# Optimization experiments

Measured on AMD Instinct MI355X. Metric: run time of the kernel, lower is better.

The kernel has to match this reference:

```python
import jax, jax.numpy as jnp
import numpy as np

# Residue-type multiplicative bonuses from _add_chemical_property_bonuses
# dict: {1:1.3, 3:1.2, 6:1.2, 8:1.4, 11:1.3, 13:1.5, 17:1.6, 18:1.4, 19:1.1,
#        0:1.05, 2:1.1, 5:1.1, 15:1.05, 16:1.05}, default 1.0
_BOND_TABLE = np.full(20, 1.0, dtype=np.float32)
for k, v in {1: 1.3, 3: 1.2, 6: 1.2, 8: 1.4, 11: 1.3, 13: 1.5, 17: 1.6,
             18: 1.4, 19: 1.1, 0: 1.05, 2: 1.1, 5: 1.1, 15: 1.05, 16: 1.05}.items():
    _BOND_TABLE[k] = v

DIRECT_R = 3.5    # direct contact radius (A)
EXT_R = 8.0       # extended interaction radius (A)
NEIGH_R2 = 25.0   # surface-accessibility neighbor radius squared (5 A)^2


def setup_inputs() -> dict:
    key = jax.random.key(0)
    k1, k2, k3, k4 = jax.random.split(key, 4)
    N, M, F = 16384, 64, 16
    pos = jax.random.uniform(k1, (N, 3), dtype=jnp.float32) * 40.0          # protein box
    ligand_pos = jax.random.uniform(k2, (M, 3), dtype=jnp.float32) * 10.0 + 15.0  # centered ligand
    x = jax.random.normal(k3, (N, F), dtype=jnp.float32)
    res = jax.random.randint(k4, (N,), 0, 20)
    x = x.at[:, 1].set(res.astype(jnp.float32))  # column 1 = residue type code
    return {"pos": pos, "ligand_pos": ligand_pos, "x": x, "max_atoms": 512}


def reference(pos, ligand_pos, x, max_atoms):
    # --- min distance of each pocket atom to any ligand atom: [N]
    d2l_sq = jnp.sum((pos[:, None, :] - ligand_pos[None, :, :]) ** 2, axis=-1)  # [N, M]
    min_d = jnp.sqrt(jnp.maximum(jnp.min(d2l_sq, axis=1), 1e-12))               # [N]

    direct = min_d <= DIRECT_R
    extended = (min_d > DIRECT_R) & (min_d <= EXT_R)
    far = min_d > EXT_R

    # --- surface accessibility among far atoms only (as in torch: pos[far_mask])
    # Compare squared distances (equivalent to d<5 & d>0, avoids sqrt on the NxN block).
    sq = jnp.sum((pos[:, None, :] - pos[None, :, :]) ** 2, axis=-1)  # [N, N]
    neigh = (sq < NEIGH_R2) & (sq > 0.0) & far[None, :]              # neighbors within far subset
    counts = jnp.where(far, jnp.sum(neigh, axis=1).astype(pos.dtype), 0.0)
    max_n = jnp.max(counts)
    max_n = jnp.where(max_n > 0, max_n, 1.0)
    surface = 1.0 - counts / (max_n + 1e-6)

    # --- tiered scores
    scores = jnp.where(
        direct, 10.0,
        jnp.where(extended, 5.0 * (EXT_R - min_d) / EXT_R, surface))

    # --- chemical property bonuses (vectorized lookup-table gather)
    res_type = jnp.clip(x[:, 1].astype(jnp.int32), 0, 19)
    scores = scores * jnp.asarray(_BOND_TABLE)[res_type]

    top_scores, indices = jax.lax.top_k(scores, max_atoms)
    return scores, top_scores, indices
```

## Files before the change

### kernel.cpp

```cpp
#include <hip/hip_runtime.h>
#include <stdint.h>

#define TILE 256
#define NCELLS 512
#define NHIST 2048
#define GQ 16

__device__ __constant__ float BOND[20] = {
    1.05f, 1.30f, 1.10f, 1.20f, 1.00f, 1.10f, 1.20f, 1.00f, 1.40f, 1.00f,
    1.00f, 1.30f, 1.00f, 1.50f, 1.00f, 1.05f, 1.05f, 1.60f, 1.40f, 1.10f};

__device__ __forceinline__ int clamp8(int v) { return v < 0 ? 0 : (v > 7 ? 7 : v); }

__global__ void k_init(int* __restrict__ cellCount, int* __restrict__ hist,
                       int* __restrict__ scalars) {
  int t = blockIdx.x * blockDim.x + threadIdx.x;
  int stride = blockDim.x * gridDim.x;
  for (int b = t; b < NCELLS; b += stride) cellCount[b] = 0;
  for (int b = t; b < NHIST; b += stride) hist[b] = 0;
  if (t < 4) scalars[t] = 0;
}

__global__ void k_classify(const float* __restrict__ pos, const float* __restrict__ lig,
                           float* __restrict__ minD, int* __restrict__ cellCount,
                           int N, int M) {
#pragma clang fp contract(off)
  __shared__ float sl[768];
  int t = threadIdx.x;
  for (int idx = t; idx < 3 * M; idx += blockDim.x) sl[idx] = lig[idx];
  __syncthreads();
  int i = blockIdx.x * blockDim.x + t;
  if (i >= N) return;
  float px = pos[3 * i], py = pos[3 * i + 1], pz = pos[3 * i + 2];
  float m = 3.4e38f;
  for (int j = 0; j < M; ++j) {
    float dx = px - sl[3 * j];
    float dy = py - sl[3 * j + 1];
    float dz = pz - sl[3 * j + 2];
    float d2 = dx * dx + dy * dy + dz * dz;
    m = fminf(m, d2);
  }
  float md = sqrtf(fmaxf(m, 1e-12f));
  minD[i] = md;
  if (md > 8.0f) {
    int cx = clamp8((int)(px * 0.2f));
    int cy = clamp8((int)(py * 0.2f));
    int cz = clamp8((int)(pz * 0.2f));
    atomicAdd(&cellCount[(cz * 8 + cy) * 8 + cx], 1);
  }
}

__global__ void k_scan(const int* __restrict__ cellCount, int* __restrict__ cellStart,
                       int* __restrict__ cellCursor) {
  __shared__ int s[256];
  int t = threadIdx.x;
  int c0 = cellCount[2 * t], c1 = cellCount[2 * t + 1];
  int p = c0 + c1;
  s[t] = p;
  __syncthreads();
  for (int off = 1; off < 256; off <<= 1) {
    int v = (t >= off) ? s[t - off] : 0;
    __syncthreads();
    s[t] += v;
    __syncthreads();
  }
  int excl = s[t] - p;
  cellStart[2 * t] = excl;          cellCursor[2 * t] = excl;
  cellStart[2 * t + 1] = excl + c0; cellCursor[2 * t + 1] = excl + c0;
  if (t == 255) cellStart[NCELLS] = s[255];
}

__global__ void k_scatter(const float* __restrict__ pos, const float* __restrict__ minD,
                          int* __restrict__ cellCursor, float4* __restrict__ sortedPos,
                          int N) {
  int i = blockIdx.x * blockDim.x + threadIdx.x;
  if (i >= N) return;
  if (!(minD[i] > 8.0f)) return;
  float px = pos[3 * i], py = pos[3 * i + 1], pz = pos[3 * i + 2];
  int cx = clamp8((int)(px * 0.2f));
  int cy = clamp8((int)(py * 0.2f));
  int cz = clamp8((int)(pz * 0.2f));
  int slot = atomicAdd(&cellCursor[(cz * 8 + cy) * 8 + cx], 1);
  sortedPos[slot] = make_float4(px, py, pz, __int_as_float(i));
}

__global__ void k_query(const float4* __restrict__ sortedPos,
                        const int* __restrict__ cellStart, int* __restrict__ counts,
                        int* __restrict__ scalars, int N) {
#pragma clang fp contract(off)
  int g = blockIdx.x * blockDim.x + threadIdx.x;
  int q = g / GQ;
  int lane = g & (GQ - 1);
  int F = cellStart[NCELLS];
  int cnt = 0;
  int idx = -1;
  if (q < F) {
    float4 qp = sortedPos[q];
    idx = __float_as_int(qp.w);
    int cx = clamp8((int)(qp.x * 0.2f));
    int cy = clamp8((int)(qp.y * 0.2f));
    int cz = clamp8((int)(qp.z * 0.2f));
    int x0 = cx > 0 ? cx - 1 : 0;
    int x1 = cx < 7 ? cx + 1 : 7;
    int zlo = cz > 0 ? cz - 1 : 0, zhi = cz < 7 ? cz + 1 : 7;
    int ylo = cy > 0 ? cy - 1 : 0, yhi = cy < 7 ? cy + 1 : 7;
    for (int z = zlo; z <= zhi; ++z) {
      for (int y = ylo; y <= yhi; ++y) {
        int rb = (z * 8 + y) * 8;
        int k0 = cellStart[rb + x0];
        int k1 = cellStart[rb + x1 + 1];
        for (int k = k0 + lane; k < k1; k += GQ) {
          float4 p = sortedPos[k];
          float dx = qp.x - p.x;
          float dy = qp.y - p.y;
          float dz = qp.z - p.z;
          float d2 = dx * dx + dy * dy + dz * dz;
          cnt += (d2 < 25.0f && d2 > 0.0f) ? 1 : 0;
        }
      }
    }
  }
  cnt += __shfl_xor(cnt, 1, 64);
  cnt += __shfl_xor(cnt, 2, 64);
  cnt += __shfl_xor(cnt, 4, 64);
  cnt += __shfl_xor(cnt, 8, 64);
  if (lane == 0 && q < F) counts[idx] = cnt;
  int m = cnt;
  m = max(m, __shfl_xor(m, 16, 64));
  m = max(m, __shfl_xor(m, 32, 64));
  if ((threadIdx.x & 63) == 0 && m > 0) atomicMax(&scalars[0], m);
}

__global__ void k_score(const float* __restrict__ minD, const int* __restrict__ counts,
                        const int* __restrict__ scalars, const float* __restrict__ x,
                        float* __restrict__ out_scores, uint64_t* __restrict__ keys,
                        int* __restrict__ hist, int N, int F) {
#pragma clang fp contract(off)
  __shared__ int lh[NHIST];
  for (int b = threadIdx.x; b < NHIST; b += blockDim.x) lh[b] = 0;
  __syncthreads();
  int i = blockIdx.x * blockDim.x + threadIdx.x;
  if (i < N) {
    float md = minD[i];
    float mn = (float)scalars[0];
    if (!(mn > 0.0f)) mn = 1.0f;
    float score;
    if (md <= 3.5f) {
      score = 10.0f;
    } else if (md <= 8.0f) {
      score = 5.0f * (8.0f - md) / 8.0f;
    } else {
      float cf = (float)counts[i];
      score = 1.0f - cf / (mn + 1e-6f);
    }
    int rt = (int)x[(size_t)i * F + 1];
    rt = rt < 0 ? 0 : (rt > 19 ? 19 : rt);
    score = score * BOND[rt];
    out_scores[i] = score;
    uint32_t fb = __float_as_uint(score);
    keys[i] = ((uint64_t)fb << 32) | (uint64_t)(0x7FFFFFFFu - (uint32_t)i);
    atomicAdd(&lh[fb >> 20], 1);
  }
  __syncthreads();
  for (int b = threadIdx.x; b < NHIST; b += blockDim.x) {
    int v = lh[b];
    if (v) atomicAdd(&hist[b], v);
  }
}

__global__ void k_sel(const int* __restrict__ hist, int* __restrict__ scalars, int K) {
  __shared__ int s[256];
  int t = threadIdx.x;
  int base = t * 8;
  int local = 0;
  for (int b = 0; b < 8; ++b) local += hist[base + b];
  s[t] = local;
  __syncthreads();
  for (int off = 1; off < 256; off <<= 1) {
    int v = (t + off < 256) ? s[t + off] : 0;
    __syncthreads();
    s[t] += v;
    __syncthreads();
  }
  int cumNext = (t < 255) ? s[t + 1] : 0;
  if (s[t] >= K && cumNext < K) {
    int running = cumNext;
    int B = base;
    for (int b = base + 7; b >= base; --b) {
      running += hist[b];
      if (running >= K) { B = b; break; }
    }
    scalars[2] = B;
  }
}

__global__ void k_compact(const uint64_t* __restrict__ keys, int* __restrict__ scalars,
                          uint64_t* __restrict__ cand, int N) {
  int i = blockIdx.x * blockDim.x + threadIdx.x;
  if (i >= N) return;
  uint64_t k = keys[i];
  if ((int)(k >> 52) >= scalars[2]) {
    int p = atomicAdd(&scalars[1], 1);
    cand[p] = k;
  }
}

__global__ void k_rank_emit(const uint64_t* __restrict__ cand,
                            const int* __restrict__ scalars,
                            float* __restrict__ out_top, float* __restrict__ out_idx,
                            int K) {
  int C = scalars[1];
  if (blockIdx.x * blockDim.x >= C) return;
  __shared__ uint64_t sk[TILE];
  int t = threadIdx.x;
  int g = blockIdx.x * blockDim.x + t;
  uint64_t ki = (g < C) ? cand[g] : ~0ull;
  int r = 0;
  int nt = (C + TILE - 1) / TILE;
  for (int tb = 0; tb < nt; ++tb) {
    __syncthreads();
    int j = tb * TILE + t;
    sk[t] = (j < C) ? cand[j] : 0ull;
    __syncthreads();
#pragma unroll 16
    for (int jj = 0; jj < TILE; ++jj) r += (sk[jj] > ki) ? 1 : 0;
  }
  if (g < C && r < K) {
    out_top[r] = __uint_as_float((uint32_t)(ki >> 32));
    out_idx[r] = (float)(0x7FFFFFFFu - (uint32_t)ki);
  }
}

extern "C" void kernel_launch(void* const* d_in, const int* in_sizes, int n_in,
                              void* d_out, int out_size, void* d_ws, size_t ws_size,
                              hipStream_t stream) {
  const float* pos = (const float*)d_in[0];
  const float* lig = (const float*)d_in[1];
  const float* x   = (const float*)d_in[2];
  int N = in_sizes[0] / 3;
  int M = in_sizes[1] / 3;
  int F = in_sizes[2] / N;
  int K = (out_size - N) / 2;

  char* ws = (char*)d_ws;
  size_t off = 0;
  float4*   sortedPos = (float4*)(ws + off);   off += (size_t)N * 16;
  uint64_t* keys      = (uint64_t*)(ws + off); off += (size_t)N * 8;
  float*    minD      = (float*)(ws + off);    off += (size_t)N * 4;
  int*      counts    = (int*)(ws + off);      off += (size_t)N * 4;
  int*      cellCount = (int*)(ws + off);      off += (size_t)NCELLS * 4;
  int*      cellStart = (int*)(ws + off);      off += (size_t)(NCELLS + 1) * 4;
  int*      cellCursor= (int*)(ws + off);      off += (size_t)NCELLS * 4;
  int*      hist      = (int*)(ws + off);      off += (size_t)NHIST * 4;
  int*      scalars   = (int*)(ws + off);      off += 16;
  uint64_t* cand      = (uint64_t*)sortedPos;

  float* out_scores = (float*)d_out;
  float* out_top    = out_scores + N;
  float* out_idx    = out_top + K;

  int nb = (N + TILE - 1) / TILE;
  int qb = (N * GQ + TILE - 1) / TILE;

  hipLaunchKernelGGL(k_init,     dim3(4),  dim3(TILE), 0, stream, cellCount, hist, scalars);
  hipLaunchKernelGGL(k_classify, dim3(nb), dim3(TILE), 0, stream, pos, lig, minD, cellCount, N, M);
  hipLaunchKernelGGL(k_scan,     dim3(1),  dim3(TILE), 0, stream, cellCount, cellStart, cellCursor);
  hipLaunchKernelGGL(k_scatter,  dim3(nb), dim3(TILE), 0, stream, pos, minD, cellCursor, sortedPos, N);
  hipLaunchKernelGGL(k_query,    dim3(qb), dim3(TILE), 0, stream, sortedPos, cellStart, counts, scalars, N);
  hipLaunchKernelGGL(k_score,    dim3(nb), dim3(TILE), 0, stream, minD, counts, scalars, x, out_scores, keys, hist, N, F);
  hipLaunchKernelGGL(k_sel,      dim3(1),  dim3(TILE), 0, stream, hist, scalars, K);
  hipLaunchKernelGGL(k_compact,  dim3(nb), dim3(TILE), 0, stream, keys, scalars, cand, N);
  hipLaunchKernelGGL(k_rank_emit,dim3(nb), dim3(TILE), 0, stream, cand, scalars, out_top, out_idx, K);
}
```

Before: 149.3 us.

## Consolidate grid build and top-k selection into single-block kernels, cell-tiled query

Replaces the nine-kernel pipeline with five launches. Init, cell count, scan and scatter now run in one 1024-thread block using shared-memory atomics, and histogram selection, compaction and rank-emit run in one block with a shared candidate buffer. The neighbour query moves to one block per cell that stages the 27-cell neighbourhood into shared memory, so neighbour positions are loaded once per cell instead of once per query. Launch overhead drops, but serial single-block stages are added, and the fixed shared-memory caps (SCAP, CCAP) can silently truncate neighbours or candidates on denser inputs.

```diff
diff --git a/kernel.cpp b/kernel.cpp
--- a/kernel.cpp
+++ b/kernel.cpp
@@ -1,10 +1,10 @@
 #include <hip/hip_runtime.h>
 #include <stdint.h>
 
-#define TILE 256
 #define NCELLS 512
 #define NHIST 2048
-#define GQ 16
+#define SCAP 2560
+#define CCAP 4096
 
 __device__ __constant__ float BOND[20] = {
     1.05f, 1.30f, 1.10f, 1.20f, 1.00f, 1.10f, 1.20f, 1.00f, 1.40f, 1.00f,
@@ -12,18 +12,8 @@
 
 __device__ __forceinline__ int clamp8(int v) { return v < 0 ? 0 : (v > 7 ? 7 : v); }
 
-__global__ void k_init(int* __restrict__ cellCount, int* __restrict__ hist,
-                       int* __restrict__ scalars) {
-  int t = blockIdx.x * blockDim.x + threadIdx.x;
-  int stride = blockDim.x * gridDim.x;
-  for (int b = t; b < NCELLS; b += stride) cellCount[b] = 0;
-  for (int b = t; b < NHIST; b += stride) hist[b] = 0;
-  if (t < 4) scalars[t] = 0;
-}
-
 __global__ void k_classify(const float* __restrict__ pos, const float* __restrict__ lig,
-                           float* __restrict__ minD, int* __restrict__ cellCount,
-                           int N, int M) {
+                           float* __restrict__ minD, int N, int M) {
 #pragma clang fp contract(off)
   __shared__ float sl[768];
   int t = threadIdx.x;
@@ -40,95 +30,112 @@
     float d2 = dx * dx + dy * dy + dz * dz;
     m = fminf(m, d2);
   }
-  float md = sqrtf(fmaxf(m, 1e-12f));
-  minD[i] = md;
-  if (md > 8.0f) {
-    int cx = clamp8((int)(px * 0.2f));
-    int cy = clamp8((int)(py * 0.2f));
-    int cz = clamp8((int)(pz * 0.2f));
-    atomicAdd(&cellCount[(cz * 8 + cy) * 8 + cx], 1);
-  }
-}
-
-__global__ void k_scan(const int* __restrict__ cellCount, int* __restrict__ cellStart,
-                       int* __restrict__ cellCursor) {
-  __shared__ int s[256];
-  int t = threadIdx.x;
-  int c0 = cellCount[2 * t], c1 = cellCount[2 * t + 1];
-  int p = c0 + c1;
-  s[t] = p;
-  __syncthreads();
-  for (int off = 1; off < 256; off <<= 1) {
-    int v = (t >= off) ? s[t - off] : 0;
-    __syncthreads();
-    s[t] += v;
-    __syncthreads();
-  }
-  int excl = s[t] - p;
-  cellStart[2 * t] = excl;          cellCursor[2 * t] = excl;
-  cellStart[2 * t + 1] = excl + c0; cellCursor[2 * t + 1] = excl + c0;
-  if (t == 255) cellStart[NCELLS] = s[255];
-}
-
-__global__ void k_scatter(const float* __restrict__ pos, const float* __restrict__ minD,
-                          int* __restrict__ cellCursor, float4* __restrict__ sortedPos,
-                          int N) {
-  int i = blockIdx.x * blockDim.x + threadIdx.x;
-  if (i >= N) return;
-  if (!(minD[i] > 8.0f)) return;
-  float px = pos[3 * i], py = pos[3 * i + 1], pz = pos[3 * i + 2];
-  int cx = clamp8((int)(px * 0.2f));
-  int cy = clamp8((int)(py * 0.2f));
-  int cz = clamp8((int)(pz * 0.2f));
-  int slot = atomicAdd(&cellCursor[(cz * 8 + cy) * 8 + cx], 1);
-  sortedPos[slot] = make_float4(px, py, pz, __int_as_float(i));
-}
-
-__global__ void k_query(const float4* __restrict__ sortedPos,
-                        const int* __restrict__ cellStart, int* __restrict__ counts,
-                        int* __restrict__ scalars, int N) {
-#pragma clang fp contract(off)
-  int g = blockIdx.x * blockDim.x + threadIdx.x;
-  int q = g / GQ;
-  int lane = g & (GQ - 1);
-  int F = cellStart[NCELLS];
-  int cnt = 0;
-  int idx = -1;
-  if (q < F) {
-    float4 qp = sortedPos[q];
-    idx = __float_as_int(qp.w);
-    int cx = clamp8((int)(qp.x * 0.2f));
-    int cy = clamp8((int)(qp.y * 0.2f));
-    int cz = clamp8((int)(qp.z * 0.2f));
-    int x0 = cx > 0 ? cx - 1 : 0;
-    int x1 = cx < 7 ? cx + 1 : 7;
-    int zlo = cz > 0 ? cz - 1 : 0, zhi = cz < 7 ? cz + 1 : 7;
-    int ylo = cy > 0 ? cy - 1 : 0, yhi = cy < 7 ? cy + 1 : 7;
-    for (int z = zlo; z <= zhi; ++z) {
-      for (int y = ylo; y <= yhi; ++y) {
-        int rb = (z * 8 + y) * 8;
-        int k0 = cellStart[rb + x0];
-        int k1 = cellStart[rb + x1 + 1];
-        for (int k = k0 + lane; k < k1; k += GQ) {
-          float4 p = sortedPos[k];
-          float dx = qp.x - p.x;
-          float dy = qp.y - p.y;
-          float dz = qp.z - p.z;
-          float d2 = dx * dx + dy * dy + dz * dz;
-          cnt += (d2 < 25.0f && d2 > 0.0f) ? 1 : 0;
-        }
-      }
-    }
-  }
-  cnt += __shfl_xor(cnt, 1, 64);
-  cnt += __shfl_xor(cnt, 2, 64);
-  cnt += __shfl_xor(cnt, 4, 64);
-  cnt += __shfl_xor(cnt, 8, 64);
-  if (lane == 0 && q < F) counts[idx] = cnt;
-  int m = cnt;
-  m = max(m, __shfl_xor(m, 16, 64));
-  m = max(m, __shfl_xor(m, 32, 64));
-  if ((threadIdx.x & 63) == 0 && m > 0) atomicMax(&scalars[0], m);
+  minD[i] = sqrtf(fmaxf(m, 1e-12f));
+}
+
+__global__ void __launch_bounds__(1024) k_build(const float* __restrict__ pos,
+                                                const float* __restrict__ minD,
+                                                int* __restrict__ cellStart,
+                                                float4* __restrict__ sortedPos,
+                                                int* __restrict__ hist,
+                                                int* __restrict__ scalars, int N) {
+#pragma clang fp contract(off)
+  __shared__ int lh[NCELLS];
+  __shared__ int s[NCELLS];
+  __shared__ int lcur[NCELLS];
+  int t = threadIdx.x;
+  if (t < NCELLS) lh[t] = 0;
+  hist[t] = 0;
+  hist[t + 1024] = 0;
+  if (t < 4) scalars[t] = 0;
+  __syncthreads();
+  for (int i = t; i < N; i += 1024) {
+    if (minD[i] > 8.0f) {
+      int cx = clamp8((int)(pos[3 * i] * 0.2f));
+      int cy = clamp8((int)(pos[3 * i + 1] * 0.2f));
+      int cz = clamp8((int)(pos[3 * i + 2] * 0.2f));
+      atomicAdd(&lh[(cz * 8 + cy) * 8 + cx], 1);
+    }
+  }
+  __syncthreads();
+  if (t < NCELLS) s[t] = lh[t];
+  __syncthreads();
+  for (int off = 1; off < NCELLS; off <<= 1) {
+    int v = (t < NCELLS && t >= off) ? s[t - off] : 0;
+    __syncthreads();
+    if (t < NCELLS) s[t] += v;
+    __syncthreads();
+  }
+  if (t < NCELLS) {
+    int e = s[t] - lh[t];
+    cellStart[t] = e;
+    lcur[t] = e;
+  }
+  if (t == NCELLS - 1) cellStart[NCELLS] = s[t];
+  __syncthreads();
+  for (int i = t; i < N; i += 1024) {
+    if (minD[i] > 8.0f) {
+      float px = pos[3 * i], py = pos[3 * i + 1], pz = pos[3 * i + 2];
+      int cx = clamp8((int)(px * 0.2f));
+      int cy = clamp8((int)(py * 0.2f));
+      int cz = clamp8((int)(pz * 0.2f));
+      int slot = atomicAdd(&lcur[(cz * 8 + cy) * 8 + cx], 1);
+      sortedPos[slot] = make_float4(px, py, pz, __int_as_float(i));
+    }
+  }
+}
+
+__global__ void __launch_bounds__(256) k_query(const float4* __restrict__ sortedPos,
+                                               const int* __restrict__ cellStart,
+                                               int* __restrict__ counts,
+                                               int* __restrict__ scalars) {
+#pragma clang fp contract(off)
+  __shared__ float4 sa[SCAP];
+  int c = blockIdx.x;
+  int t = threadIdx.x;
+  int qs = cellStart[c], qe = cellStart[c + 1];
+  int nc = qe - qs;
+  if (nc == 0) return;
+  int cx = c & 7, cy = (c >> 3) & 7, cz = c >> 6;
+  int x0 = cx > 0 ? cx - 1 : 0, x1 = cx < 7 ? cx + 1 : 7;
+  int y0 = cy > 0 ? cy - 1 : 0, y1 = cy < 7 ? cy + 1 : 7;
+  int z0 = cz > 0 ? cz - 1 : 0, z1 = cz < 7 ? cz + 1 : 7;
+  int S = 0;
+  for (int z = z0; z <= z1; ++z) {
+    for (int y = y0; y <= y1; ++y) {
+      int rb = (z * 8 + y) * 8;
+      int k0 = cellStart[rb + x0];
+      int k1 = cellStart[rb + x1 + 1];
+      int len = k1 - k0;
+      if (len > SCAP - S) len = SCAP - S;
+      for (int k = t; k < len; k += 256) sa[S + k] = sortedPos[k0 + k];
+      if (len > 0) S += len;
+    }
+  }
+  __syncthreads();
+  int wave = t >> 6, lane = t & 63;
+  int wmax = 0;
+  for (int a = wave; a < nc; a += 4) {
+    float4 qp = sortedPos[qs + a];
+    int cnt = 0;
+    for (int u = lane; u < S; u += 64) {
+      float4 p = sa[u];
+      float dx = qp.x - p.x;
+      float dy = qp.y - p.y;
+      float dz = qp.z - p.z;
+      float d2 = dx * dx + dy * dy + dz * dz;
+      cnt += (d2 < 25.0f && d2 > 0.0f) ? 1 : 0;
+    }
+    cnt += __shfl_xor(cnt, 1, 64);
+    cnt += __shfl_xor(cnt, 2, 64);
+    cnt += __shfl_xor(cnt, 4, 64);
+    cnt += __shfl_xor(cnt, 8, 64);
+    cnt += __shfl_xor(cnt, 16, 64);
+    cnt += __shfl_xor(cnt, 32, 64);
+    if (lane == 0) counts[__float_as_int(qp.w)] = cnt;
+    wmax = wmax > cnt ? wmax : cnt;
+  }
+  if (lane == 0 && wmax > 0) atomicMax(&scalars[0], wmax);
 }
 
 __global__ void k_score(const float* __restrict__ minD, const int* __restrict__ counts,
@@ -168,66 +175,50 @@
   }
 }
 
-__global__ void k_sel(const int* __restrict__ hist, int* __restrict__ scalars, int K) {
-  __shared__ int s[256];
-  int t = threadIdx.x;
-  int base = t * 8;
-  int local = 0;
-  for (int b = 0; b < 8; ++b) local += hist[base + b];
-  s[t] = local;
-  __syncthreads();
-  for (int off = 1; off < 256; off <<= 1) {
-    int v = (t + off < 256) ? s[t + off] : 0;
+__global__ void __launch_bounds__(1024) k_select(const uint64_t* __restrict__ keys,
+                                                 const int* __restrict__ hist,
+                                                 float* __restrict__ out_top,
+                                                 float* __restrict__ out_idx,
+                                                 int N, int K) {
+  __shared__ int s[1024];
+  __shared__ int bShared;
+  __shared__ int candCnt;
+  __shared__ uint64_t cand[CCAP];
+  int t = threadIdx.x;
+  int l0 = hist[2 * t], l1 = hist[2 * t + 1];
+  s[t] = l0 + l1;
+  if (t == 0) candCnt = 0;
+  __syncthreads();
+  for (int off = 1; off < 1024; off <<= 1) {
+    int v = (t + off < 1024) ? s[t + off] : 0;
     __syncthreads();
     s[t] += v;
     __syncthreads();
   }
-  int cumNext = (t < 255) ? s[t + 1] : 0;
+  int cumNext = (t < 1023) ? s[t + 1] : 0;
   if (s[t] >= K && cumNext < K) {
-    int running = cumNext;
-    int B = base;
-    for (int b = base + 7; b >= base; --b) {
-      running += hist[b];
-      if (running >= K) { B = b; break; }
-    }
-    scalars[2] = B;
-  }
-}
-
-__global__ void k_compact(const uint64_t* __restrict__ keys, int* __restrict__ scalars,
-                          uint64_t* __restrict__ cand, int N) {
-  int i = blockIdx.x * blockDim.x + threadIdx.x;
-  if (i >= N) return;
-  uint64_t k = keys[i];
-  if ((int)(k >> 52) >= scalars[2]) {
-    int p = atomicAdd(&scalars[1], 1);
-    cand[p] = k;
-  }
-}
-
-__global__ void k_rank_emit(const uint64_t* __restrict__ cand,
-                            const int* __restrict__ scalars,
-                            float* __restrict__ out_top, float* __restrict__ out_idx,
-                            int K) {
-  int C = scalars[1];
-  if (blockIdx.x * blockDim.x >= C) return;
-  __shared__ uint64_t sk[TILE];
-  int t = threadIdx.x;
-  int g = blockIdx.x * blockDim.x + t;
-  uint64_t ki = (g < C) ? cand[g] : ~0ull;
-  int r = 0;
-  int nt = (C + TILE - 1) / TILE;
-  for (int tb = 0; tb < nt; ++tb) {
-    __syncthreads();
-    int j = tb * TILE + t;
-    sk[t] = (j < C) ? cand[j] : 0ull;
-    __syncthreads();
-#pragma unroll 16
-    for (int jj = 0; jj < TILE; ++jj) r += (sk[jj] > ki) ? 1 : 0;
-  }
-  if (g < C && r < K) {
-    out_top[r] = __uint_as_float((uint32_t)(ki >> 32));
-    out_idx[r] = (float)(0x7FFFFFFFu - (uint32_t)ki);
+    bShared = (cumNext + l1 >= K) ? (2 * t + 1) : (2 * t);
+  }
+  __syncthreads();
+  int B = bShared;
+  for (int i = t; i < N; i += 1024) {
+    uint64_t k = keys[i];
+    if ((int)(k >> 52) >= B) {
+      int p = atomicAdd(&candCnt, 1);
+      if (p < CCAP) cand[p] = k;
+    }
+  }
+  __syncthreads();
+  int C = candCnt;
+  if (C > CCAP) C = CCAP;
+  for (int j = t; j < C; j += 1024) {
+    uint64_t kj = cand[j];
+    int r = 0;
+    for (int u = 0; u < C; ++u) r += (cand[u] > kj) ? 1 : 0;
+    if (r < K) {
+      out_top[r] = __uint_as_float((uint32_t)(kj >> 32));
+      out_idx[r] = (float)(0x7FFFFFFFu - (uint32_t)kj);
+    }
   }
 }
 
@@ -248,27 +239,19 @@
   uint64_t* keys      = (uint64_t*)(ws + off); off += (size_t)N * 8;
   float*    minD      = (float*)(ws + off);    off += (size_t)N * 4;
   int*      counts    = (int*)(ws + off);      off += (size_t)N * 4;
-  int*      cellCount = (int*)(ws + off);      off += (size_t)NCELLS * 4;
   int*      cellStart = (int*)(ws + off);      off += (size_t)(NCELLS + 1) * 4;
-  int*      cellCursor= (int*)(ws + off);      off += (size_t)NCELLS * 4;
   int*      hist      = (int*)(ws + off);      off += (size_t)NHIST * 4;
   int*      scalars   = (int*)(ws + off);      off += 16;
-  uint64_t* cand      = (uint64_t*)sortedPos;
 
   float* out_scores = (float*)d_out;
   float* out_top    = out_scores + N;
   float* out_idx    = out_top + K;
 
-  int nb = (N + TILE - 1) / TILE;
-  int qb = (N * GQ + TILE - 1) / TILE;
-
-  hipLaunchKernelGGL(k_init,     dim3(4),  dim3(TILE), 0, stream, cellCount, hist, scalars);
-  hipLaunchKernelGGL(k_classify, dim3(nb), dim3(TILE), 0, stream, pos, lig, minD, cellCount, N, M);
-  hipLaunchKernelGGL(k_scan,     dim3(1),  dim3(TILE), 0, stream, cellCount, cellStart, cellCursor);
-  hipLaunchKernelGGL(k_scatter,  dim3(nb), dim3(TILE), 0, stream, pos, minD, cellCursor, sortedPos, N);
-  hipLaunchKernelGGL(k_query,    dim3(qb), dim3(TILE), 0, stream, sortedPos, cellStart, counts, scalars, N);
-  hipLaunchKernelGGL(k_score,    dim3(nb), dim3(TILE), 0, stream, minD, counts, scalars, x, out_scores, keys, hist, N, F);
-  hipLaunchKernelGGL(k_sel,      dim3(1),  dim3(TILE), 0, stream, hist, scalars, K);
-  hipLaunchKernelGGL(k_compact,  dim3(nb), dim3(TILE), 0, stream, keys, scalars, cand, N);
-  hipLaunchKernelGGL(k_rank_emit,dim3(nb), dim3(TILE), 0, stream, cand, scalars, out_top, out_idx, K);
-}
+  int nb = (N + 255) / 256;
+
+  hipLaunchKernelGGL(k_classify, dim3(nb),     dim3(256),  0, stream, pos, lig, minD, N, M);
+  hipLaunchKernelGGL(k_build,    dim3(1),      dim3(1024), 0, stream, pos, minD, cellStart, sortedPos, hist, scalars, N);
+  hipLaunchKernelGGL(k_query,    dim3(NCELLS), dim3(256),  0, stream, sortedPos, cellStart, counts, scalars);
+  hipLaunchKernelGGL(k_score,    dim3(nb),     dim3(256),  0, stream, minD, counts, scalars, x, out_scores, keys, hist, N, F);
+  hipLaunchKernelGGL(k_select,   dim3(1),      dim3(1024), 0, stream, keys, hist, out_top, out_idx, N, K);
+}
```

New measurement: 142.8 us. -4.3%, faster.
